# Kernel optimization log

Hardware: AMD Instinct MI355X
Metric: run time of the kernel (lower is better)

Reference implementation:

```python
import jax, jax.numpy as jnp
import numpy as np

B, T, C, HS, WS = 16, 16, 128, 32, 32

def _conv1x1(w, b, t):
    # w: [Cout, Cin], t: [B, Cin, H, W] -> [B, Cout, H, W]
    return jnp.einsum('oi,bihw->bohw', w, t) + b[None, :, None, None]

def setup_inputs() -> dict:
    key = jax.random.key(0)
    ks = jax.random.split(key, 6)
    x = jax.random.normal(ks[0], (B, T, C, HS, WS), dtype=jnp.float32)
    c0 = jax.random.normal(ks[1], (B, C, HS, WS), dtype=jnp.float32) * 1e-6
    # conv1..conv5: Cin=C; conv6..conv13: Cin=2C
    W5 = jax.random.normal(ks[2], (5, C, C), dtype=jnp.float32) * 0.05
    b5 = jax.random.normal(ks[3], (5, C), dtype=jnp.float32) * 0.05
    W8 = jax.random.normal(ks[4], (8, C, 2 * C), dtype=jnp.float32) * 0.05
    b8 = jax.random.normal(ks[5], (8, C), dtype=jnp.float32) * 0.05
    return {"x": x, "c0": c0, "W5": W5, "b5": b5, "W8": W8, "b8": b8}

def _self_attention_memory(W5, b5, W8, b8, m, h):
    vh = _conv1x1(W5[0], b5[0], h)            # conv1
    kh = _conv1x1(W5[1], b5[1], h)            # conv2
    qh = _conv1x1(W5[2], b5[2], h)            # conv3
    qh = jnp.swapaxes(qh, 2, 3)               # transpose spatial (needs H==W)
    ah = jax.nn.softmax(kh * qh, axis=-1)
    zh = vh * ah
    km = _conv1x1(W5[3], b5[3], m)            # conv4
    vm = _conv1x1(W5[4], b5[4], m)            # conv5
    am = jax.nn.softmax(qh * km, axis=-1)
    zm = vm * am
    z = _conv1x1(W8[0], b8[0], jnp.concatenate((zh, zm), axis=1))  # conv6
    hz = jnp.concatenate((h, z), axis=1)
    ot = jax.nn.sigmoid(_conv1x1(W8[1], b8[1], hz))   # conv7
    gt = jnp.tanh(_conv1x1(W8[2], b8[2], hz))         # conv8
    it = jax.nn.sigmoid(_conv1x1(W8[3], b8[3], hz))   # conv9
    mt = gt * it + (1.0 - it) * m
    ht = ot * mt
    return mt, ht

def _forward(x, c0, W5, b5, W8, b8):
    xt = jnp.transpose(x, (1, 0, 2, 3, 4))   # [T, B, C, H, W]
    mem0 = jnp.zeros_like(xt[0])
    h0 = jnp.zeros_like(xt[0])

    def step(carry, xi):
        mem, H, Cst = carry
        hx = jnp.concatenate((H, xi), axis=1)
        a_xh = jax.nn.sigmoid(_conv1x1(W8[4], b8[4], hx))   # conv10
        ga = jax.nn.sigmoid(_conv1x1(W8[5], b8[5], hx))     # conv11
        gv = jnp.tanh(_conv1x1(W8[6], b8[6], hx))           # conv12
        Cst = Cst * a_xh + ga * gv
        a_xh1 = jax.nn.sigmoid(_conv1x1(W8[7], b8[7], hx))  # conv13
        H = a_xh1 * jnp.tanh(Cst)
        mem, H = _self_attention_memory(W5, b5, W8, b8, mem, H)
        return (mem, H, Cst), None

    (mem, H, Cst), _ = jax.lax.scan(step, (mem0, h0, c0), xt)
    return H

def reference(x, c0, W5, b5, W8, b8):
    return _forward(x, c0, W5, b5, W8, b8)
```

## Files before the change

kernel.cpp:

```cpp
#include <hip/hip_runtime.h>
#include <hip/hip_bf16.h>

#define BB 16
#define TT 16
#define CC 128
#define HW 1024
#define PIX (CC*HW)
#define STOT ((long)BB*PIX)

#define TW16 4096
#define WI16 131072
#define WZ16 262144
#define XW16 2097152

typedef short short8 __attribute__((ext_vector_type(8)));
typedef float f32x4  __attribute__((ext_vector_type(4)));

__device__ __forceinline__ float sigf(float x) { return 1.0f / (1.0f + __expf(-x)); }
__device__ __forceinline__ float tanhf_fast(float x) {
    float ax = fabsf(x);
    float t = __expf(-2.0f * ax);
    float r = (1.0f - t) / (1.0f + t);
    return copysignf(r, x);
}

__device__ __forceinline__ unsigned short pack_bf16(float x) {
    unsigned u = __float_as_uint(x);
    return (unsigned short)((u + 0x7fffu + ((u >> 16) & 1u)) >> 16);
}
__device__ __forceinline__ float bf16f(unsigned short s) {
    return __uint_as_float(((unsigned)s) << 16);
}

__device__ __forceinline__ long bidx16(int p, int c, int nkt) {
    int kb = (c >> 3) & 3;
    int phys = ((p & 127) + (kb << 4)) & 127;
    return ((long)((p >> 7) * nkt + (c >> 5)) << 12) + (kb << 10) + (phys << 3) + (c & 7);
}

typedef __attribute__((address_space(3))) unsigned lds_u32_t;
typedef __attribute__((address_space(1))) const unsigned gbl_u32_t;
__device__ __forceinline__ void gld16(const void* g, unsigned* l) {
    __builtin_amdgcn_global_load_lds((gbl_u32_t*)g, (lds_u32_t*)l, 16, 0, 0);
}

template<int MODE>
__global__ __launch_bounds__(256, 2) void gemm_mfma(
    const unsigned short* __restrict__ Wp, const float* __restrict__ bias,
    const unsigned short* __restrict__ imgA, long wA,
    const unsigned short* __restrict__ imgB, long wB, int nktB,
    int k_split, int m_split,
    void* __restrict__ outv, void* __restrict__ stv,
    unsigned short* __restrict__ simg, float* __restrict__ Hout,
    int M, int K)
{
    __shared__ __align__(16) unsigned As[2][4096];
    __shared__ __align__(16) unsigned Bs[2][4096];

    const int b  = blockIdx.z;
    const int n0 = blockIdx.x * 128;
    const int m0 = blockIdx.y * 128;
    const int t  = threadIdx.x;
    const int lane = t & 63;
    const int w  = t >> 6;
    const int wm = w & 1, wn = w >> 1;
    const int g  = lane >> 4, pl = lane & 15;
    const int nk64 = K >> 6;

    f32x4 acc[4][4] = {};

    auto stageA = [&](int kchunk, unsigned* dst) {
        const char* gA = (const char*)(Wp +
            (size_t)((m0 >> 7) * (K >> 5) + (kchunk >> 5)) * TW16);
        gld16(gA + t * 16, dst + t * 4);
        gld16(gA + 4096 + t * 16, dst + 1024 + t * 4);
    };
    auto stageB = [&](int kchunk, unsigned* dst) {
        const bool useB = (m0 >= m_split) || (kchunk >= k_split);
        const int kc = useB ? (kchunk - ((m0 >= m_split) ? 0 : k_split)) : kchunk;
        const unsigned short* img = useB ? imgB : imgA;
        const long bw = useB ? wB : wA;
        const int nkt = useB ? nktB : 4;
        const char* gB = (const char*)(img + (long)b * bw +
            ((long)((n0 >> 7) * nkt + (kc >> 5)) << 12));
        gld16(gB + t * 16, dst + t * 4);
        gld16(gB + 4096 + t * 16, dst + 1024 + t * 4);
    };
    auto stage = [&](int k0, int buf) {
        stageA(k0,      As[buf]);
        stageA(k0 + 32, As[buf] + 2048);
        stageB(k0,      Bs[buf]);
        stageB(k0 + 32, Bs[buf] + 2048);
    };

    stage(0, 0);

    for (int it = 0; it < nk64; ++it) {
        const int buf = it & 1;
        __syncthreads();
        if (it + 1 < nk64) stage((it + 1) << 6, buf ^ 1);

        #pragma unroll
        for (int h = 0; h < 2; ++h) {
            short8 afr[4], bfr[4];
            #pragma unroll
            for (int mt = 0; mt < 4; ++mt) {
                int row = 64 * wm + 16 * mt + pl;
                int phys = (row + (g << 4)) & 127;
                afr[mt] = *(const short8*)((const char*)As[buf] + h * 8192 + g * 2048 + phys * 16);
            }
            #pragma unroll
            for (int nt = 0; nt < 4; ++nt) {
                int prow = 64 * wn + 16 * nt + pl;
                int phys = (prow + (g << 4)) & 127;
                bfr[nt] = *(const short8*)((const char*)Bs[buf] + h * 8192 + g * 2048 + phys * 16);
            }
            #pragma unroll
            for (int mt = 0; mt < 4; ++mt)
                #pragma unroll
                for (int nt = 0; nt < 4; ++nt)
                    acc[mt][nt] = __builtin_amdgcn_mfma_f32_16x16x32_bf16(afr[mt], bfr[nt], acc[mt][nt], 0, 0, 0);
        }
    }

    if (MODE == 1) {
        #pragma unroll
        for (int mt = 0; mt < 4; ++mt)
            #pragma unroll
            for (int r = 0; r < 4; ++r) {
                int row = m0 + 64 * wm + 16 * mt + 4 * g + r;
                float bb = bias[row];
                #pragma unroll
                for (int nt = 0; nt < 4; ++nt) {
                    int col = n0 + 64 * wn + 16 * nt + pl;
                    ((unsigned short*)outv)[((long)b * M + row) * HW + col] =
                        pack_bf16(acc[mt][nt][r] + bb);
                }
            }
    } else {
        const float4* bias4 = (const float4*)bias;
        unsigned short* Hp = (unsigned short*)outv;
        #pragma unroll
        for (int mt = 0; mt < 4; ++mt) {
            int c = (m0 >> 2) + 16 * wm + 4 * mt + g;
            float4 bb = bias4[c];
            #pragma unroll
            for (int nt = 0; nt < 4; ++nt) {
                int p = n0 + 64 * wn + 16 * nt + pl;
                long lidx = (long)b * PIX + (long)c * HW + p;
                long widx = (long)b * WI16 + bidx16(p, c, 4);
                float v0 = acc[mt][nt][0] + bb.x;
                float v1 = acc[mt][nt][1] + bb.y;
                float v2 = acc[mt][nt][2] + bb.z;
                float v3 = acc[mt][nt][3] + bb.w;
                if (MODE == 2) {
                    float* Cst = (float*)stv;
                    float cc = Cst[lidx] * sigf(v0) + sigf(v1) * tanhf_fast(v2);
                    Cst[lidx] = cc;
                    Hp[widx] = pack_bf16(sigf(v3) * tanhf_fast(cc));
                } else {
                    float* mpf = (float*)stv;
                    float ot = sigf(v0), gt = tanhf_fast(v1), it2 = sigf(v2);
                    float mo = mpf[lidx];
                    float mn = gt * it2 + (1.0f - it2) * mo;
                    mpf[lidx] = mn;
                    simg[widx] = pack_bf16(mn);
                    float hv = ot * mn;
                    Hp[widx] = pack_bf16(hv);
                    if (Hout) Hout[lidx] = hv;
                }
            }
        }
    }
}

__global__ __launch_bounds__(1024) void attn_kernel(
    const unsigned short* __restrict__ VKM, unsigned short* __restrict__ Zimg)
{
    __shared__ float qs[4][32 * 33];
    const int tid = threadIdx.x;
    const int b = blockIdx.x >> 5, cq = blockIdx.x & 31;
    const int c0 = cq << 2;
    const long base = (long)b * 640 * HW;

    #pragma unroll
    for (int cc = 0; cc < 4; ++cc)
        qs[cc][(tid >> 5) * 33 + (tid & 31)] =
            bf16f(VKM[base + (long)(256 + c0 + cc) * HW + tid]);
    __syncthreads();

    const int i = tid >> 5, j = tid & 31;
    unsigned short zh[4], zm[4];
    #pragma unroll
    for (int cc = 0; cc < 4; ++cc) {
        const long cbs = base + (long)(c0 + cc) * HW;
        float qhT = qs[cc][j * 33 + i];
        float vh  = bf16f(VKM[cbs + tid]);
        float kh  = bf16f(VKM[cbs + 128l * HW + tid]);
        float km  = bf16f(VKM[cbs + 384l * HW + tid]);
        float vm  = bf16f(VKM[cbs + 512l * HW + tid]);

        float sh = kh * qhT, sm = qhT * km;
        float mh = sh, mm = sm;
        #pragma unroll
        for (int o = 16; o > 0; o >>= 1) {
            mh = fmaxf(mh, __shfl_xor(mh, o, 32));
            mm = fmaxf(mm, __shfl_xor(mm, o, 32));
        }
        float eh = __expf(sh - mh), em = __expf(sm - mm);
        float s1 = eh, s2 = em;
        #pragma unroll
        for (int o = 16; o > 0; o >>= 1) {
            s1 += __shfl_xor(s1, o, 32);
            s2 += __shfl_xor(s2, o, 32);
        }
        zh[cc] = pack_bf16(vh * (eh / s1));
        zm[cc] = pack_bf16(vm * (em / s2));
    }
    const int kt = c0 >> 5, kb = (c0 >> 3) & 3, sl = c0 & 7;
    const int phys = ((tid & 127) + (kb << 4)) & 127;
    long e16 = (long)b * WZ16 + ((long)((tid >> 7) * 8 + kt) << 12) +
               (kb << 10) + (phys << 3) + sl;
    uint2 oh, om;
    oh.x = (unsigned)zh[0] | ((unsigned)zh[1] << 16);
    oh.y = (unsigned)zh[2] | ((unsigned)zh[3] << 16);
    om.x = (unsigned)zm[0] | ((unsigned)zm[1] << 16);
    om.y = (unsigned)zm[2] | ((unsigned)zm[3] << 16);
    *(uint2*)(Zimg + e16)              = oh;
    *(uint2*)(Zimg + e16 + (4l << 12)) = om;
}

__global__ __launch_bounds__(256) void pack_x(
    const float* __restrict__ x, uint4* __restrict__ Xp, int tstart, int oneshot)
{
    long q = (long)blockIdx.x * 256 + threadIdx.x;
    long e = q << 3;
    int t = tstart + (int)(e >> 21);
    long r = e & ((1l << 21) - 1);
    int b = (int)(r >> 17);
    int v = (int)(r & ((1 << 17) - 1));
    int tile = v >> 12;
    int pt = tile >> 2, kt = tile & 3;
    int ww = v & 4095;
    int kb = ww >> 10, phys = (ww >> 3) & 127;
    int row = (phys - (kb << 4)) & 127;
    int p = (pt << 7) + row;
    int c = (kt << 5) + (kb << 3);
    const float* xs = x + (((long)b * TT + t) * CC + c) * HW + p;
    union { unsigned short s[8]; uint4 u; } o;
    #pragma unroll
    for (int jj = 0; jj < 8; ++jj)
        o.s[jj] = pack_bf16(xs[(long)jj * HW]);
    Xp[oneshot ? q : (q & ((1l << 18) - 1))] = o.u;
}

__device__ __forceinline__ void wimg(unsigned short* img, int Ktiles, int r, int k, float v) {
    int tile = (r >> 7) * Ktiles + (k >> 5);
    int row = r & 127, ks = k & 31;
    int kb = ks >> 3;
    int phys = (row + (kb << 4)) & 127;
    img[(size_t)tile * TW16 + (kb << 10) + (phys << 3) + (ks & 7)] = pack_bf16(v);
}

__global__ __launch_bounds__(256) void setup_all(
    const float* __restrict__ W5, const float* __restrict__ W8, const float* __restrict__ b8,
    unsigned short* __restrict__ Wp5i,
    unsigned short* __restrict__ Wgi, float* __restrict__ bg4,
    unsigned short* __restrict__ Woi, float* __restrict__ bo4)
{
    int idx = blockIdx.x * 256 + threadIdx.x;
    if (idx < 81920) {
        int r = idx >> 7, k = idx & 127;
        wimg(Wp5i, 4, r, k, W5[idx]);
        return;
    }
    idx -= 81920;
    if (idx < 131072) {
        int rr = idx >> 8, k = idx & 255;
        int c = rr >> 2, gg = rr & 3;
        wimg(Wgi, 8, rr, k, W8[((long)(4 + gg) * 128 + c) * 256 + k]);
        if (k == 0) bg4[rr] = b8[(4 + gg) * 128 + c];
        return;
    }
    idx -= 131072;
    if (idx >= 512 * 384) return;
    int rr = idx / 384, k = idx - rr * 384;
    int c = rr >> 2, gg = rr & 3;
    float wv = 0.0f;
    if (gg < 3) {
        const float* wr = W8 + ((long)(1 + gg) * 128 + c) * 256;
        if (k < 128) {
            wv = wr[k];
        } else {
            int i = k - 128;
            float s = 0.0f;
            for (int j = 0; j < 128; ++j)
                s += wr[128 + j] * W8[(long)j * 256 + i];
            wv = s;
        }
    }
    wimg(Woi, 12, rr, k, wv);
    if (k == 0) {
        float bb = 0.0f;
        if (gg < 3) {
            bb = b8[(1 + gg) * 128 + c];
            const float* wr = W8 + ((long)(1 + gg) * 128 + c) * 256;
            for (int j = 0; j < 128; ++j) bb += wr[128 + j] * b8[j];
        }
        bo4[rr] = bb;
    }
}

extern "C" void kernel_launch(void* const* d_in, const int* in_sizes, int n_in,
                              void* d_out, int out_size, void* d_ws, size_t ws_size,
                              hipStream_t stream)
{
    const float* x  = (const float*)d_in[0];
    const float* c0 = (const float*)d_in[1];
    const float* W5 = (const float*)d_in[2];
    const float* b5 = (const float*)d_in[3];
    const float* W8 = (const float*)d_in[4];
    const float* b8 = (const float*)d_in[5];
    float* out = (float*)d_out;

    const long S = STOT;
    unsigned short* Ha  = (unsigned short*)d_ws;
    unsigned short* Hb  = Ha + 16l * WI16;
    unsigned short* mpi = Hb + 16l * WI16;
    float* mpf = (float*)(mpi + 16l * WI16);
    float* Cst = mpf + S;
    unsigned short* Wp5i = (unsigned short*)(Cst + S);
    unsigned short* Wgi  = Wp5i + 20 * TW16;
    unsigned short* Woi  = Wgi + 32 * TW16;
    float* bg4 = (float*)(Woi + 48 * TW16);
    float* bo4 = bg4 + 512;
    unsigned short* VKM  = (unsigned short*)(bo4 + 512);
    unsigned short* Zimg = VKM + 5 * S;
    unsigned short* Xp   = Zimg + 16l * WZ16;

    const bool havex =
        ((char*)(Xp + 16l * XW16) - (char*)d_ws) <= (long)ws_size;

    hipMemsetAsync(Hb,  0, 16l * WI16 * 2, stream);
    hipMemsetAsync(mpi, 0, 16l * WI16 * 2, stream);
    hipMemsetAsync(mpf, 0, S * sizeof(float), stream);
    hipMemcpyAsync(Cst, c0, S * sizeof(float), hipMemcpyDeviceToDevice, stream);

    setup_all<<<1600, dim3(256), 0, stream>>>(W5, W8, b8, Wp5i, Wgi, bg4, Woi, bo4);
    if (havex)
        pack_x<<<16384, dim3(256), 0, stream>>>(x, (uint4*)Xp, 0, 1);

    const int BIG = 1 << 30;
    const dim3 blk(256);
    for (int t = 0; t < TT; ++t) {
        if (!havex)
            pack_x<<<1024, dim3(256), 0, stream>>>(x, (uint4*)Xp, t, 0);
        const unsigned short* Xpt = Xp + (havex ? (long)t * XW16 : 0l);

        gemm_mfma<2><<<dim3(8, 4, 16), blk, 0, stream>>>(
            Wgi, bg4, Hb, (long)WI16, Xpt, (long)WI16, 4,
            128, BIG, Ha, Cst, nullptr, nullptr, 512, 256);

        gemm_mfma<1><<<dim3(8, 5, 16), blk, 0, stream>>>(
            Wp5i, b5, Ha, (long)WI16, mpi, (long)WI16, 4,
            BIG, 384, VKM, nullptr, nullptr, nullptr, 640, 128);

        attn_kernel<<<512, dim3(1024), 0, stream>>>(VKM, Zimg);

        gemm_mfma<3><<<dim3(8, 4, 16), blk, 0, stream>>>(
            Woi, bo4, Ha, (long)WI16, Zimg, (long)WZ16, 8,
            128, BIG, Hb, mpf, mpi, (t == TT - 1) ? out : nullptr, 512, 384);
    }
}
```

Baseline: 1.085 ms.

## Store VKM channel-quad interleaved and process 8 channels per attention block

The MODE 1 GEMM epilogue now writes its bf16 output with four consecutive channels packed into one 8-byte word per pixel, instead of scattering single 2-byte stores. The attention kernel reads that layout with 8-byte loads, handles 8 channels per block instead of 4, and writes 16-byte Z stores, with half as many blocks. The aim is to cut the number of narrow global memory transactions in both kernels. In exchange, per-thread register use and LDS size grow (8 transposed q tiles), and the VKM layout contract between the two kernels changes.

```diff
diff --git a/kernel.cpp b/kernel.cpp
--- a/kernel.cpp
+++ b/kernel.cpp
@@ -28,8 +28,8 @@
     unsigned u = __float_as_uint(x);
     return (unsigned short)((u + 0x7fffu + ((u >> 16) & 1u)) >> 16);
 }
-__device__ __forceinline__ float bf16f(unsigned short s) {
-    return __uint_as_float(((unsigned)s) << 16);
+__device__ __forceinline__ float bf16f(unsigned s) {
+    return __uint_as_float(s << 16);
 }
 
 __device__ __forceinline__ long bidx16(int p, int c, int nkt) {
@@ -124,19 +124,23 @@
     }
 
     if (MODE == 1) {
+        const float4* b4 = (const float4*)bias;
+        uint2* V2 = (uint2*)outv;
         #pragma unroll
-        for (int mt = 0; mt < 4; ++mt)
+        for (int mt = 0; mt < 4; ++mt) {
+            int rq = (m0 >> 2) + 16 * wm + 4 * mt + g;
+            float4 bb = b4[rq];
             #pragma unroll
-            for (int r = 0; r < 4; ++r) {
-                int row = m0 + 64 * wm + 16 * mt + 4 * g + r;
-                float bb = bias[row];
-                #pragma unroll
-                for (int nt = 0; nt < 4; ++nt) {
-                    int col = n0 + 64 * wn + 16 * nt + pl;
-                    ((unsigned short*)outv)[((long)b * M + row) * HW + col] =
-                        pack_bf16(acc[mt][nt][r] + bb);
-                }
+            for (int nt = 0; nt < 4; ++nt) {
+                int col = n0 + 64 * wn + 16 * nt + pl;
+                uint2 o;
+                o.x = (unsigned)pack_bf16(acc[mt][nt][0] + bb.x) |
+                      ((unsigned)pack_bf16(acc[mt][nt][1] + bb.y) << 16);
+                o.y = (unsigned)pack_bf16(acc[mt][nt][2] + bb.z) |
+                      ((unsigned)pack_bf16(acc[mt][nt][3] + bb.w) << 16);
+                V2[((long)b * (M >> 2) + rq) * 1024 + col] = o;
             }
+        }
     } else {
         const float4* bias4 = (const float4*)bias;
         unsigned short* Hp = (unsigned short*)outv;
@@ -175,32 +179,53 @@
 }
 
 __global__ __launch_bounds__(1024) void attn_kernel(
-    const unsigned short* __restrict__ VKM, unsigned short* __restrict__ Zimg)
+    const uint2* __restrict__ VKM2, uint4* __restrict__ Zimg4)
 {
-    __shared__ float qs[4][32 * 33];
+    __shared__ float qs[8][32 * 33];
     const int tid = threadIdx.x;
-    const int b = blockIdx.x >> 5, cq = blockIdx.x & 31;
-    const int c0 = cq << 2;
-    const long base = (long)b * 640 * HW;
-
+    const int b = blockIdx.x >> 4, c8 = blockIdx.x & 15;
+    const int c0 = c8 << 3;
+    const int q0 = c8 << 1;
+    const long pb = (long)b * 160 * 1024;
+
+    {
+        uint2 qa = VKM2[pb + (long)(64 + q0) * 1024 + tid];
+        uint2 qb = VKM2[pb + (long)(65 + q0) * 1024 + tid];
+        int ti = (tid & 31) * 33 + (tid >> 5);
+        qs[0][ti] = bf16f(qa.x & 0xffffu); qs[1][ti] = bf16f(qa.x >> 16);
+        qs[2][ti] = bf16f(qa.y & 0xffffu); qs[3][ti] = bf16f(qa.y >> 16);
+        qs[4][ti] = bf16f(qb.x & 0xffffu); qs[5][ti] = bf16f(qb.x >> 16);
+        qs[6][ti] = bf16f(qb.y & 0xffffu); qs[7][ti] = bf16f(qb.y >> 16);
+    }
+    __syncthreads();
+
+    float vh[8], kh[8], km[8], vm[8];
+    {
+        uint2 a, c;
+        a = VKM2[pb + (long)(0 + q0) * 1024 + tid];
+        c = VKM2[pb + (long)(1 + q0) * 1024 + tid];
+        vh[0]=bf16f(a.x&0xffffu); vh[1]=bf16f(a.x>>16); vh[2]=bf16f(a.y&0xffffu); vh[3]=bf16f(a.y>>16);
+        vh[4]=bf16f(c.x&0xffffu); vh[5]=bf16f(c.x>>16); vh[6]=bf16f(c.y&0xffffu); vh[7]=bf16f(c.y>>16);
+        a = VKM2[pb + (long)(32 + q0) * 1024 + tid];
+        c = VKM2[pb + (long)(33 + q0) * 1024 + tid];
+        kh[0]=bf16f(a.x&0xffffu); kh[1]=bf16f(a.x>>16); kh[2]=bf16f(a.y&0xffffu); kh[3]=bf16f(a.y>>16);
+        kh[4]=bf16f(c.x&0xffffu); kh[5]=bf16f(c.x>>16); kh[6]=bf16f(c.y&0xffffu); kh[7]=bf16f(c.y>>16);
+        a = VKM2[pb + (long)(96 + q0) * 1024 + tid];
+        c = VKM2[pb + (long)(97 + q0) * 1024 + tid];
+        km[0]=bf16f(a.x&0xffffu); km[1]=bf16f(a.x>>16); km[2]=bf16f(a.y&0xffffu); km[3]=bf16f(a.y>>16);
+        km[4]=bf16f(c.x&0xffffu); km[5]=bf16f(c.x>>16); km[6]=bf16f(c.y&0xffffu); km[7]=bf16f(c.y>>16);
+        a = VKM2[pb + (long)(128 + q0) * 1024 + tid];
+        c = VKM2[pb + (long)(129 + q0) * 1024 + tid];
+        vm[0]=bf16f(a.x&0xffffu); vm[1]=bf16f(a.x>>16); vm[2]=bf16f(a.y&0xffffu); vm[3]=bf16f(a.y>>16);
+        vm[4]=bf16f(c.x&0xffffu); vm[5]=bf16f(c.x>>16); vm[6]=bf16f(c.y&0xffffu); vm[7]=bf16f(c.y>>16);
+    }
+
+    unsigned short zh[8], zm[8];
+    const int ti = (tid >> 5) * 33 + (tid & 31);
     #pragma unroll
-    for (int cc = 0; cc < 4; ++cc)
-        qs[cc][(tid >> 5) * 33 + (tid & 31)] =
-            bf16f(VKM[base + (long)(256 + c0 + cc) * HW + tid]);
-    __syncthreads();
-
-    const int i = tid >> 5, j = tid & 31;
-    unsigned short zh[4], zm[4];
-    #pragma unroll
-    for (int cc = 0; cc < 4; ++cc) {
-        const long cbs = base + (long)(c0 + cc) * HW;
-        float qhT = qs[cc][j * 33 + i];
-        float vh  = bf16f(VKM[cbs + tid]);
-        float kh  = bf16f(VKM[cbs + 128l * HW + tid]);
-        float km  = bf16f(VKM[cbs + 384l * HW + tid]);
-        float vm  = bf16f(VKM[cbs + 512l * HW + tid]);
-
-        float sh = kh * qhT, sm = qhT * km;
+    for (int cc = 0; cc < 8; ++cc) {
+        float qhT = qs[cc][ti];
+        float sh = kh[cc] * qhT, sm = qhT * km[cc];
         float mh = sh, mm = sm;
         #pragma unroll
         for (int o = 16; o > 0; o >>= 1) {
@@ -214,20 +239,24 @@
             s1 += __shfl_xor(s1, o, 32);
             s2 += __shfl_xor(s2, o, 32);
         }
-        zh[cc] = pack_bf16(vh * (eh / s1));
-        zm[cc] = pack_bf16(vm * (em / s2));
-    }
-    const int kt = c0 >> 5, kb = (c0 >> 3) & 3, sl = c0 & 7;
+        zh[cc] = pack_bf16(vh[cc] * (eh / s1));
+        zm[cc] = pack_bf16(vm[cc] * (em / s2));
+    }
+    const int kt = c0 >> 5, kb = (c0 >> 3) & 3;
     const int phys = ((tid & 127) + (kb << 4)) & 127;
     long e16 = (long)b * WZ16 + ((long)((tid >> 7) * 8 + kt) << 12) +
-               (kb << 10) + (phys << 3) + sl;
-    uint2 oh, om;
+               (kb << 10) + (phys << 3);
+    uint4 oh, om;
     oh.x = (unsigned)zh[0] | ((unsigned)zh[1] << 16);
     oh.y = (unsigned)zh[2] | ((unsigned)zh[3] << 16);
+    oh.z = (unsigned)zh[4] | ((unsigned)zh[5] << 16);
+    oh.w = (unsigned)zh[6] | ((unsigned)zh[7] << 16);
     om.x = (unsigned)zm[0] | ((unsigned)zm[1] << 16);
     om.y = (unsigned)zm[2] | ((unsigned)zm[3] << 16);
-    *(uint2*)(Zimg + e16)              = oh;
-    *(uint2*)(Zimg + e16 + (4l << 12)) = om;
+    om.z = (unsigned)zm[4] | ((unsigned)zm[5] << 16);
+    om.w = (unsigned)zm[6] | ((unsigned)zm[7] << 16);
+    Zimg4[e16 >> 3]                 = oh;
+    Zimg4[(e16 + (4l << 12)) >> 3]  = om;
 }
 
 __global__ __launch_bounds__(256) void pack_x(
@@ -365,7 +394,7 @@
             Wp5i, b5, Ha, (long)WI16, mpi, (long)WI16, 4,
             BIG, 384, VKM, nullptr, nullptr, nullptr, 640, 128);
 
-        attn_kernel<<<512, dim3(1024), 0, stream>>>(VKM, Zimg);
+        attn_kernel<<<256, dim3(1024), 0, stream>>>((const uint2*)VKM, (uint4*)Zimg);
 
         gemm_mfma<3><<<dim3(8, 4, 16), blk, 0, stream>>>(
             Woi, bo4, Ha, (long)WI16, Zimg, (long)WZ16, 8,
```

Result: faster. 1.050 ms (-3.3%).
